# Performance work log

Hardware: AMD Instinct MI355X
Metric: run time of the kernel (lower is better)

## Reference

```python
import math
import jax, jax.numpy as jnp
import numpy as np

D_MODEL = 512
NHEAD = 8
D_HEAD = D_MODEL // NHEAD
TEMP = 0.8
B, LQ, LK = 16, 512, 1024
NEG = -1.0e9


def setup_inputs() -> dict:
    key = jax.random.key(0)
    ks = jax.random.split(key, 12)
    s = 1.0 / math.sqrt(D_MODEL)
    return {
        "Q_src": jax.random.normal(ks[0], (B, LQ, D_MODEL), jnp.float32),
        "KV_src": jax.random.normal(ks[1], (B, LK, D_MODEL), jnp.float32),
        "key_gate": jax.random.uniform(ks[2], (B, LK), jnp.float32, 1e-3, 1.0),
        "key_padding_mask": jax.random.randint(ks[3], (B, LK), 0, 2, jnp.int32),
        "Wq": jax.random.normal(ks[4], (D_MODEL, D_MODEL), jnp.float32) * s,
        "bq": jnp.zeros((D_MODEL,), jnp.float32),
        "Wk": jax.random.normal(ks[5], (D_MODEL, D_MODEL), jnp.float32) * s,
        "bk": jnp.zeros((D_MODEL,), jnp.float32),
        "Wv": jax.random.normal(ks[6], (D_MODEL, D_MODEL), jnp.float32) * s,
        "bv": jnp.zeros((D_MODEL,), jnp.float32),
        "Wo": jax.random.normal(ks[7], (D_MODEL, D_MODEL), jnp.float32) * s,
        "bo": jnp.zeros((D_MODEL,), jnp.float32),
    }


def reference(Q_src, KV_src, key_gate, key_padding_mask, Wq, bq, Wk, bk, Wv, bv, Wo, bo):
    b, lq, _ = Q_src.shape
    lk = KV_src.shape[1]
    # projections -> [B, H, L, Dh]
    q = (Q_src @ Wq + bq).reshape(b, lq, NHEAD, D_HEAD).transpose(0, 2, 1, 3)
    k = (KV_src @ Wk + bk).reshape(b, lk, NHEAD, D_HEAD).transpose(0, 2, 1, 3)
    v = (KV_src @ Wv + bv).reshape(b, lk, NHEAD, D_HEAD).transpose(0, 2, 1, 3)
    # scores with log-gate bias [B, H, Lq, Lk]
    logits = jnp.einsum("bhqd,bhkd->bhqk", q, k) / math.sqrt(D_HEAD)
    logits = logits + jnp.log(key_gate)[:, None, None, :]
    pad = (key_padding_mask == 0)[:, None, None, :]
    logits = jnp.where(pad, NEG, logits) / TEMP
    attn = jax.nn.softmax(logits, axis=-1)
    ctx = jnp.einsum("bhqk,bhkd->bhqd", attn, v)
    ctx = ctx.transpose(0, 2, 1, 3).reshape(b, lq, D_MODEL)
    return ctx @ Wo + bo
```

## Files before the change

kernel.cpp:

```cpp
#include <hip/hip_runtime.h>
#include <math.h>

typedef __bf16 bf16;
typedef __bf16 bf16x8 __attribute__((ext_vector_type(8)));
typedef __bf16 bf16x4 __attribute__((ext_vector_type(4)));
typedef __bf16 bf16x2 __attribute__((ext_vector_type(2)));
typedef float  f32x4  __attribute__((ext_vector_type(4)));
typedef unsigned int uint;

#define SCQ2 0.22542110f
#define SMREF 16.0f

#define VMC(n) asm volatile("s_waitcnt vmcnt(" #n ")" ::: "memory")
#define BARR do { __builtin_amdgcn_s_barrier(); __builtin_amdgcn_sched_barrier(0); } while (0)

#if __has_builtin(__builtin_amdgcn_exp2f)
#define EXP2F __builtin_amdgcn_exp2f
#else
#define EXP2F exp2f
#endif

__device__ __forceinline__ void gload16(const void* g, void* l) {
  __builtin_amdgcn_global_load_lds((const __attribute__((address_space(1))) void*)g,
                                   (__attribute__((address_space(3))) void*)l, 16, 0, 0);
}

__device__ __forceinline__ uint pk2(float a, float b) {
  bf16x2 t = {(bf16)a, (bf16)b};
  return __builtin_bit_cast(uint, t);
}

union V8 { bf16x8 v; bf16x4 h[2]; uint u[4]; };

__global__ void prep_k(const float* __restrict__ Wq, const float* __restrict__ Wk,
                       const float* __restrict__ Wv, const float* __restrict__ Wo,
                       bf16* __restrict__ Tq, bf16* __restrict__ Tkv, bf16* __restrict__ To,
                       const float* __restrict__ gate, const int* __restrict__ mask,
                       float* __restrict__ gfac,
                       const float* __restrict__ Qs, const float* __restrict__ KVs,
                       bf16* __restrict__ Qsb, bf16* __restrict__ KVb) {
  const int bid = blockIdx.x, tid = threadIdx.x;
  if (bid < 256) {
    const int w = bid >> 6, t = bid & 63;
    const float* W = (w == 0) ? Wq : (w == 1) ? Wk : (w == 2) ? Wv : Wo;
    bf16* T = (w == 0) ? Tq : (w == 3) ? To : Tkv;
    const int ro = (w == 2) ? 512 : 0;
    const int k0 = (t >> 3) * 64, n0 = (t & 7) * 64;
    __shared__ bf16 tl[64][72];
#pragma unroll
    for (int i = 0; i < 16; i++) {
      int s = i * 256 + tid;
      int r = s >> 6, c = s & 63;
      tl[r][c] = (bf16)W[(size_t)(k0 + r) * 512 + n0 + c];
    }
    __syncthreads();
#pragma unroll
    for (int i = 0; i < 16; i++) {
      int s = i * 256 + tid;
      int r = s >> 6, c = s & 63;
      T[(size_t)(ro + n0 + r) * 512 + k0 + c] = tl[c][r];
    }
  } else if (bid < 320) {
    int i = (bid - 256) * 256 + tid;
    gfac[i] = mask[i] ? __expf(1.25f * __logf(gate[i])) : 0.0f;
  } else {
    const float* s;
    bf16* d;
    size_t i;
    if (bid < 2368) { s = Qs; d = Qsb; i = ((size_t)(bid - 320) * 256 + tid) * 8; }
    else            { s = KVs; d = KVb; i = ((size_t)(bid - 2368) * 256 + tid) * 8; }
    f32x4 a = *(const f32x4*)(s + i);
    f32x4 b = *(const f32x4*)(s + i + 4);
    bf16x8 o = {(bf16)a[0], (bf16)a[1], (bf16)a[2], (bf16)a[3],
                (bf16)b[0], (bf16)b[1], (bf16)b[2], (bf16)b[3]};
    *(bf16x8*)(d + i) = o;
  }
}

__global__ __launch_bounds__(512, 2) void gemm_kv8(
    const bf16* __restrict__ A, const bf16* __restrict__ Bt,
    const float* __restrict__ kb, const float* __restrict__ vb,
    const float* __restrict__ gfac, bf16* __restrict__ K_out, bf16* __restrict__ V_out) {
  const int tid = threadIdx.x, w = tid >> 6, l = tid & 63;
  const int lg = l >> 4, lr = l & 15;
  const int bid = (int)(blockIdx.x & 7) * 32 + (int)(blockIdx.x >> 3);
  const int bm = (bid >> 2) * 256;
  const int bn = (bid & 3) * 256;
  const int wm = w >> 2, wn = w & 3;

  __shared__ __align__(16) bf16 AB[2][16384];

  const int lrow = l >> 2;
  const int cs = (l & 3) ^ ((l >> 3) & 3);

  f32x4 acc[8][4];
#pragma unroll
  for (int i = 0; i < 8; i++)
#pragma unroll
    for (int j = 0; j < 4; j++) acc[i][j] = (f32x4){0.f, 0.f, 0.f, 0.f};

  auto stA = [&](int p, int u, int kt) {
    const int rb = (w >> 2) * 128 + u * 64 + (w & 3) * 16;
    gload16(A + (size_t)(bm + rb + lrow) * 512 + kt * 32 + cs * 8, &AB[p][rb * 32]);
  };
  auto stB = [&](int p, int u, int kt) {
    const int rb = (w >> 1) * 64 + u * 32 + (w & 1) * 16;
    gload16(Bt + (size_t)(bn + rb + lrow) * 512 + kt * 32 + cs * 8, &AB[p][8192 + rb * 32]);
  };

  bf16x8 aA[4], bb0[2], bb1[2];
#define RDA(p, mh)                                                                   \
  _Pragma("unroll") for (int m2 = 0; m2 < 4; m2++) {                                 \
    const int row = wm * 128 + (mh) * 64 + m2 * 16 + lr;                             \
    aA[m2] = *(const bf16x8*)(&AB[p][row * 32 + ((lg ^ ((row >> 1) & 3)) * 8)]);     \
  }
#define RDB(p, nh, dst)                                                              \
  _Pragma("unroll") for (int n2 = 0; n2 < 2; n2++) {                                 \
    const int row = wn * 64 + (nh) * 32 + n2 * 16 + lr;                              \
    dst[n2] = *(const bf16x8*)(&AB[p][8192 + row * 32 + ((lg ^ ((row >> 1) & 3)) * 8)]); \
  }
#define MM(mh, nh, bbv)                                                              \
  __builtin_amdgcn_s_setprio(1);                                                     \
  _Pragma("unroll") for (int m2 = 0; m2 < 4; m2++)                                   \
  _Pragma("unroll") for (int n2 = 0; n2 < 2; n2++)                                   \
    acc[(mh) * 4 + m2][(nh) * 2 + n2] =                                              \
        __builtin_amdgcn_mfma_f32_16x16x32_bf16(aA[m2], bbv[n2],                     \
                                                acc[(mh) * 4 + m2][(nh) * 2 + n2], 0, 0, 0); \
  __builtin_amdgcn_s_setprio(0);

  stA(0, 0, 0); stB(0, 0, 0); stA(0, 1, 0); stB(0, 1, 0);
  stA(1, 0, 1); stB(1, 0, 1);
  VMC(4);
  BARR;

  for (int i = 0; i < 8; ++i) {
    const bool last = (i == 7);
    const int k1 = 2 * i + 1, k2 = 2 * i + 2, k3 = 2 * i + 3;
    stA(1, 1, k1); stB(1, 1, k1);
    RDA(0, 0); RDB(0, 0, bb0);
    MM(0, 0, bb0);
    VMC(4); BARR;
    RDB(0, 1, bb1);
    MM(0, 1, bb1);
    BARR;
    if (!last) stA(0, 0, k2);
    RDA(0, 1);
    MM(1, 0, bb0);
    BARR;
    if (!last) stB(0, 0, k2);
    MM(1, 1, bb1);
    if (last) { VMC(2); } else { VMC(4); }
    BARR;
    if (!last) { stA(0, 1, k2); stB(0, 1, k2); }
    RDA(1, 0); RDB(1, 0, bb0);
    MM(0, 0, bb0);
    if (last) { VMC(0); } else { VMC(4); }
    BARR;
    RDB(1, 1, bb1);
    MM(0, 1, bb1);
    BARR;
    if (!last) stA(1, 0, k3);
    RDA(1, 1);
    MM(1, 0, bb0);
    BARR;
    if (!last) stB(1, 0, k3);
    MM(1, 1, bb1);
    VMC(4); BARR;
  }
#undef RDA
#undef RDB
#undef MM

  if (bn < 512) {
#pragma unroll
    for (int mf = 0; mf < 8; mf++) {
#pragma unroll
      for (int nf = 0; nf < 4; nf++) {
        f32x4 c = acc[mf][nf];
        const int n = bn + wn * 64 + nf * 16 + lr;
        const int m0 = bm + wm * 128 + mf * 16 + lg * 4;
        const float bias = kb[n];
#pragma unroll
        for (int r = 0; r < 4; r++) K_out[(size_t)(m0 + r) * 512 + n] = (bf16)(c[r] + bias);
      }
    }
  } else {
#pragma unroll
    for (int mf = 0; mf < 8; mf++) {
#pragma unroll
      for (int nf = 0; nf < 4; nf++) {
        f32x4 c = acc[mf][nf];
        const int n = bn + wn * 64 + nf * 16 + lr;
        const int m0 = bm + wm * 128 + mf * 16 + lg * 4;
        const int nn = n - 512;
        const int hh = nn >> 6, dd = nn & 63;
        const int bb = m0 >> 10, key = m0 & 1023;
        const int u = key & 31;
        const int keyp = (key & ~31) + ((u & 15) >> 2) * 8 + ((u >> 4) & 1) * 4;
        const float bias = vb[nn];
        f32x4 g4 = *(const f32x4*)(gfac + m0);
        bf16x4 w4 = {(bf16)((c[0] + bias) * g4[0]), (bf16)((c[1] + bias) * g4[1]),
                     (bf16)((c[2] + bias) * g4[2]), (bf16)((c[3] + bias) * g4[3])};
        *(bf16x4*)(V_out + ((size_t)((bb * 8 + hh) * 64 + dd)) * 1024 + keyp) = w4;
      }
    }
  }
}

template <int OM, int NT, int CHUNK>
__global__ __launch_bounds__(256, 2) void gemm_k(
    const bf16* __restrict__ A, const bf16* __restrict__ Bt,
    const float* __restrict__ b0, void* __restrict__ C0, float scale) {
  const int tid = threadIdx.x, w = tid >> 6, l = tid & 63;
  const int lg = l >> 4, lr = l & 15;
  const int bid = (int)(blockIdx.x & 7) * CHUNK + (int)(blockIdx.x >> 3);
  const int bm = (bid / NT) * 64;
  const int bn = (bid % NT) * 128;
  const int wr = (w >> 1) * 32, wc = (w & 1) * 64;
  __shared__ __align__(16) bf16 As[3][64][32];
  __shared__ __align__(16) bf16 Bs[3][128][32];
  const int r16 = l >> 2;
  const int cs = (l & 3) ^ ((l >> 3) & 3);

  f32x4 acc[2][4];
#pragma unroll
  for (int i = 0; i < 2; i++)
#pragma unroll
    for (int j = 0; j < 4; j++) acc[i][j] = (f32x4){0.f, 0.f, 0.f, 0.f};

  auto stage = [&](int buf, int kt) {
    gload16(A + (size_t)(bm + w * 16 + r16) * 512 + kt * 32 + cs * 8, &As[buf][w * 16][0]);
#pragma unroll
    for (int j = 0; j < 2; j++)
      gload16(Bt + (size_t)(bn + w * 32 + j * 16 + r16) * 512 + kt * 32 + cs * 8,
              &Bs[buf][w * 32 + j * 16][0]);
  };

  stage(0, 0);
  stage(1, 1);
  for (int t = 0; t < 16; ++t) {
    const int buf = t % 3;
    if (t == 15) { VMC(0); } else { VMC(3); }
    BARR;
    if (t < 14) stage((t + 2) % 3, t + 2);
    bf16x8 af[2], bfr[4];
#pragma unroll
    for (int mf = 0; mf < 2; mf++) {
      const int row = wr + mf * 16 + lr;
      af[mf] = *(const bf16x8*)(&As[buf][row][(lg ^ ((row >> 1) & 3)) * 8]);
    }
#pragma unroll
    for (int nf = 0; nf < 4; nf++) {
      const int row = wc + nf * 16 + lr;
      bfr[nf] = *(const bf16x8*)(&Bs[buf][row][(lg ^ ((row >> 1) & 3)) * 8]);
    }
    __builtin_amdgcn_s_setprio(1);
#pragma unroll
    for (int mf = 0; mf < 2; mf++)
#pragma unroll
      for (int nf = 0; nf < 4; nf++)
        acc[mf][nf] = __builtin_amdgcn_mfma_f32_16x16x32_bf16(af[mf], bfr[nf], acc[mf][nf], 0, 0, 0);
    __builtin_amdgcn_s_setprio(0);
  }

#pragma unroll
  for (int mf = 0; mf < 2; mf++) {
#pragma unroll
    for (int nf = 0; nf < 4; nf++) {
      f32x4 c = acc[mf][nf];
      const int n = bn + wc + nf * 16 + lr;
      const int m0 = bm + wr + mf * 16 + lg * 4;
      const float bias = b0[n];
      if constexpr (OM == 0) {
        bf16* C = (bf16*)C0;
#pragma unroll
        for (int r = 0; r < 4; r++) C[(size_t)(m0 + r) * 512 + n] = (bf16)((c[r] + bias) * scale);
      } else {
        float* C = (float*)C0;
#pragma unroll
        for (int r = 0; r < 4; r++) C[(size_t)(m0 + r) * 512 + n] = c[r] + bias;
      }
    }
  }
}

__global__ __launch_bounds__(512, 1) void attn_k(
    const bf16* __restrict__ Q, const bf16* __restrict__ Kb,
    const bf16* __restrict__ Vt, const float* __restrict__ gfac,
    bf16* __restrict__ ctx) {
  const int tid = threadIdx.x, w = tid >> 6, l = tid & 63;
  const int lg = l >> 4, lr = l & 15;
  const int ks = w >> 2, wl = w & 3;
  const int bid = (int)(blockIdx.x & 7) * 32 + (int)(blockIdx.x >> 3);
  const int qb = bid & 1, h = (bid >> 1) & 7, b = bid >> 4;
  const int q0 = qb * 256;

  __shared__ __align__(16) bf16 Ks[2][2][64][64];
  __shared__ __align__(16) bf16 Vs[2][2][64][64];
  __shared__ __align__(16) float gfs[1024];

  bf16x8 qf[4][2];
#pragma unroll
  for (int s = 0; s < 4; s++) {
    const bf16* qp = Q + (size_t)(b * 512 + q0 + wl * 64 + s * 16 + lr) * 512 + h * 64;
    qf[s][0] = *(const bf16x8*)(qp + lg * 8);
    qf[s][1] = *(const bf16x8*)(qp + 32 + lg * 8);
  }

  f32x4 o[4][4];
#pragma unroll
  for (int s = 0; s < 4; s++)
#pragma unroll
    for (int i = 0; i < 4; i++) o[s][i] = (f32x4){0.f, 0.f, 0.f, 0.f};
  f32x4 lacc[4] = {(f32x4){0.f, 0.f, 0.f, 0.f}, (f32x4){0.f, 0.f, 0.f, 0.f},
                   (f32x4){0.f, 0.f, 0.f, 0.f}, (f32x4){0.f, 0.f, 0.f, 0.f}};

  const int r8 = l >> 3;
  const int c8g = (l & 7) ^ ((l >> 3) & 7);
  const bf16* Kbase = Kb + ((size_t)b * 1024) * 512 + h * 64 + c8g * 8;
  const bf16* Vbase = Vt + ((size_t)(b * 8 + h) * 64) * 1024 + c8g * 8;

  auto stage = [&](int buf, int t) {
    const int kv0 = ks * 512 + t * 64;
    gload16(Kbase + (size_t)(kv0 + wl * 16 + r8) * 512, &Ks[ks][buf][wl * 16][0]);
    gload16(Kbase + (size_t)(kv0 + wl * 16 + 8 + r8) * 512, &Ks[ks][buf][wl * 16 + 8][0]);
    gload16(Vbase + (size_t)(wl * 16 + r8) * 1024 + kv0, &Vs[ks][buf][wl * 16][0]);
    gload16(Vbase + (size_t)(wl * 16 + 8 + r8) * 1024 + kv0, &Vs[ks][buf][wl * 16 + 8][0]);
  };

  if (w < 4) gload16(gfac + b * 1024 + w * 256 + l * 4, &gfs[w * 256]);
  stage(0, 0);

  for (int t = 0; t < 8; ++t) {
    const int buf = t & 1;
    VMC(0);
    BARR;
    if (t < 7) stage(buf ^ 1, t + 1);

    f32x4 gvv[4];
#pragma unroll
    for (int f = 0; f < 4; f++)
      gvv[f] = *(const f32x4*)(&gfs[ks * 512 + t * 64 + f * 16 + lg * 4]);

    bf16x8 kf[4][2];
#pragma unroll
    for (int f = 0; f < 4; f++) {
      const int row = f * 16 + lr;
      kf[f][0] = *(const bf16x8*)(&Ks[ks][buf][row][(lg ^ (row & 7)) * 8]);
      kf[f][1] = *(const bf16x8*)(&Ks[ks][buf][row][((4 + lg) ^ (row & 7)) * 8]);
    }

    V8 pb[4][2];
#pragma unroll
    for (int s = 0; s < 4; s++) {
      f32x4 s4[4];
      __builtin_amdgcn_s_setprio(1);
#pragma unroll
      for (int f = 0; f < 4; f++) {
        f32x4 z = (f32x4){-SMREF, -SMREF, -SMREF, -SMREF};
        z = __builtin_amdgcn_mfma_f32_16x16x32_bf16(kf[f][0], qf[s][0], z, 0, 0, 0);
        s4[f] = __builtin_amdgcn_mfma_f32_16x16x32_bf16(kf[f][1], qf[s][1], z, 0, 0, 0);
      }
      __builtin_amdgcn_s_setprio(0);
      float p[4][4];
#pragma unroll
      for (int f = 0; f < 4; f++)
#pragma unroll
        for (int r = 0; r < 4; r++) p[f][r] = EXP2F(s4[f][r]);
#pragma unroll
      for (int f = 0; f < 4; f++)
#pragma unroll
        for (int r = 0; r < 4; r++) lacc[s][r] = fmaf(p[f][r], gvv[f][r], lacc[s][r]);
      pb[s][0].u[0] = pk2(p[0][0], p[0][1]); pb[s][0].u[1] = pk2(p[0][2], p[0][3]);
      pb[s][0].u[2] = pk2(p[1][0], p[1][1]); pb[s][0].u[3] = pk2(p[1][2], p[1][3]);
      pb[s][1].u[0] = pk2(p[2][0], p[2][1]); pb[s][1].u[1] = pk2(p[2][2], p[2][3]);
      pb[s][1].u[2] = pk2(p[3][0], p[3][1]); pb[s][1].u[3] = pk2(p[3][2], p[3][3]);
    }

    __builtin_amdgcn_s_setprio(1);
#pragma unroll
    for (int od = 0; od < 4; od++) {
      const int row = od * 16 + lr;
      const bf16x8 va0 = *(const bf16x8*)(&Vs[ks][buf][row][(lg ^ (row & 7)) * 8]);
      const bf16x8 va1 = *(const bf16x8*)(&Vs[ks][buf][row][((4 + lg) ^ (row & 7)) * 8]);
#pragma unroll
      for (int s = 0; s < 4; s++) {
        o[s][od] = __builtin_amdgcn_mfma_f32_16x16x32_bf16(va0, pb[s][0].v, o[s][od], 0, 0, 0);
        o[s][od] = __builtin_amdgcn_mfma_f32_16x16x32_bf16(va1, pb[s][1].v, o[s][od], 0, 0, 0);
      }
    }
    __builtin_amdgcn_s_setprio(0);
  }

  f32x4* OmA = (f32x4*)&Ks[0][0][0][0];
  f32x4* OmB = (f32x4*)&Vs[0][0][0][0];
  float* Lp = (float*)gfs;
  __syncthreads();
  if (ks == 1) {
    const int base = (wl * 64 + l) * 8;
#pragma unroll
    for (int s = 0; s < 2; s++)
#pragma unroll
      for (int od = 0; od < 4; od++) OmA[base + ((s * 4 + od) ^ (l & 7))] = o[s][od];
#pragma unroll
    for (int s = 2; s < 4; s++)
#pragma unroll
      for (int od = 0; od < 4; od++) OmB[base + (((s - 2) * 4 + od) ^ (l & 7))] = o[s][od];
#pragma unroll
    for (int s = 0; s < 4; s++)
      Lp[(wl * 64 + l) * 4 + s] = (lacc[s][0] + lacc[s][1]) + (lacc[s][2] + lacc[s][3]);
  }
  __syncthreads();
  if (ks == 0) {
    const int base = (wl * 64 + l) * 8;
#pragma unroll
    for (int s = 0; s < 2; s++)
#pragma unroll
      for (int od = 0; od < 4; od++) o[s][od] += OmA[base + ((s * 4 + od) ^ (l & 7))];
#pragma unroll
    for (int s = 2; s < 4; s++)
#pragma unroll
      for (int od = 0; od < 4; od++) o[s][od] += OmB[base + (((s - 2) * 4 + od) ^ (l & 7))];
#pragma unroll
    for (int s = 0; s < 4; s++) {
      float lp = (lacc[s][0] + lacc[s][1]) + (lacc[s][2] + lacc[s][3]) +
                 Lp[(wl * 64 + l) * 4 + s];
      lp += __shfl_xor(lp, 16);
      lp += __shfl_xor(lp, 32);
      const float inv = 1.0f / lp;
      bf16* cp = ctx + (size_t)(b * 512 + q0 + wl * 64 + s * 16 + lr) * 512 + h * 64;
#pragma unroll
      for (int od = 0; od < 4; od++)
#pragma unroll
        for (int r = 0; r < 4; r++) cp[od * 16 + lg * 4 + r] = (bf16)(o[s][od][r] * inv);
    }
  }
}

extern "C" void kernel_launch(void* const* d_in, const int* in_sizes, int n_in,
                              void* d_out, int out_size, void* d_ws, size_t ws_size,
                              hipStream_t stream) {
  (void)in_sizes; (void)n_in; (void)out_size; (void)ws_size;
  const float* Q_src = (const float*)d_in[0];
  const float* KV_src = (const float*)d_in[1];
  const float* gate = (const float*)d_in[2];
  const int* mask = (const int*)d_in[3];
  const float* Wq = (const float*)d_in[4];
  const float* bq = (const float*)d_in[5];
  const float* Wk = (const float*)d_in[6];
  const float* bk = (const float*)d_in[7];
  const float* Wv = (const float*)d_in[8];
  const float* bv = (const float*)d_in[9];
  const float* Wo = (const float*)d_in[10];
  const float* bo = (const float*)d_in[11];
  float* out = (float*)d_out;

  char* ws = (char*)d_ws;
  size_t off = 0;
  auto alloc = [&](size_t bytes) {
    char* p = ws + off;
    off += (bytes + 255) & ~(size_t)255;
    return p;
  };
  bf16* Wtq = (bf16*)alloc(512 * 512 * 2);
  bf16* Btkv = (bf16*)alloc(1024 * 512 * 2);
  bf16* Wto = (bf16*)alloc(512 * 512 * 2);
  float* gfac = (float*)alloc(16384 * 4);
  bf16* Qsb = (bf16*)alloc((size_t)8192 * 512 * 2);
  bf16* KVb = (bf16*)alloc((size_t)16384 * 512 * 2);
  bf16* Qb = (bf16*)alloc((size_t)8192 * 512 * 2);
  bf16* Kb = (bf16*)alloc((size_t)16384 * 512 * 2);
  bf16* Vt = (bf16*)alloc((size_t)16384 * 512 * 2);
  bf16* Cx = KVb;

  prep_k<<<6464, 256, 0, stream>>>(Wq, Wk, Wv, Wo, Wtq, Btkv, Wto, gate, mask, gfac,
                                   Q_src, KV_src, Qsb, KVb);
  gemm_kv8<<<256, 512, 0, stream>>>(KVb, Btkv, bk, bv, gfac, Kb, Vt);
  gemm_k<0, 4, 64><<<512, 256, 0, stream>>>(Qsb, Wtq, bq, Qb, SCQ2);
  attn_k<<<256, 512, 0, stream>>>(Qb, Kb, Vt, gfac, Cx);
  gemm_k<2, 4, 64><<<512, 256, 0, stream>>>(Cx, Wto, bo, out, 1.0f);
}
```

Before: 86.19 us.

## Load K/V fragments directly from global into registers, drop LDS staging

Removes the LDS double-buffered K/V staging with per-iteration barriers. Each wave now reads its K and V MFMA fragments straight from global memory into registers, with K prefetched one tile ahead and the gate factors also read from global. Launch bounds are changed to allow two blocks per CU. In exchange, the four query-row waves sharing a kv-split now each fetch the same K/V data, so traffic relies on L1/L2 hits, and register pressure rises from the doubled K buffer plus V fragments under the tighter launch bound.

```diff
diff --git a/kernel.cpp b/kernel.cpp
--- a/kernel.cpp
+++ b/kernel.cpp
@@ -284,7 +284,7 @@
   }
 }
 
-__global__ __launch_bounds__(512, 1) void attn_k(
+__global__ __launch_bounds__(512, 2) void attn_k(
     const bf16* __restrict__ Q, const bf16* __restrict__ Kb,
     const bf16* __restrict__ Vt, const float* __restrict__ gfac,
     bf16* __restrict__ ctx) {
@@ -295,9 +295,9 @@
   const int qb = bid & 1, h = (bid >> 1) & 7, b = bid >> 4;
   const int q0 = qb * 256;
 
-  __shared__ __align__(16) bf16 Ks[2][2][64][64];
-  __shared__ __align__(16) bf16 Vs[2][2][64][64];
-  __shared__ __align__(16) float gfs[1024];
+  __shared__ __align__(16) f32x4 OmA[2048];
+  __shared__ __align__(16) f32x4 OmB[2048];
+  __shared__ __align__(16) float Lp[1024];
 
   bf16x8 qf[4][2];
 #pragma unroll
@@ -315,40 +315,35 @@
   f32x4 lacc[4] = {(f32x4){0.f, 0.f, 0.f, 0.f}, (f32x4){0.f, 0.f, 0.f, 0.f},
                    (f32x4){0.f, 0.f, 0.f, 0.f}, (f32x4){0.f, 0.f, 0.f, 0.f}};
 
-  const int r8 = l >> 3;
-  const int c8g = (l & 7) ^ ((l >> 3) & 7);
-  const bf16* Kbase = Kb + ((size_t)b * 1024) * 512 + h * 64 + c8g * 8;
-  const bf16* Vbase = Vt + ((size_t)(b * 8 + h) * 64) * 1024 + c8g * 8;
-
-  auto stage = [&](int buf, int t) {
-    const int kv0 = ks * 512 + t * 64;
-    gload16(Kbase + (size_t)(kv0 + wl * 16 + r8) * 512, &Ks[ks][buf][wl * 16][0]);
-    gload16(Kbase + (size_t)(kv0 + wl * 16 + 8 + r8) * 512, &Ks[ks][buf][wl * 16 + 8][0]);
-    gload16(Vbase + (size_t)(wl * 16 + r8) * 1024 + kv0, &Vs[ks][buf][wl * 16][0]);
-    gload16(Vbase + (size_t)(wl * 16 + 8 + r8) * 1024 + kv0, &Vs[ks][buf][wl * 16 + 8][0]);
+  const bf16* Kbh = Kb + ((size_t)(b * 1024 + ks * 512)) * 512 + h * 64;
+  const bf16* Vbh = Vt + ((size_t)(b * 8 + h) * 64) * 1024 + ks * 512;
+  const float* gbh = gfac + b * 1024 + ks * 512;
+
+  bf16x8 kf[2][4][2];
+  auto loadK = [&](int t, int buf) {
+#pragma unroll
+    for (int f = 0; f < 4; f++) {
+      const size_t ro = (size_t)(t * 64 + f * 16 + lr) * 512;
+      kf[buf][f][0] = *(const bf16x8*)(Kbh + ro + lg * 8);
+      kf[buf][f][1] = *(const bf16x8*)(Kbh + ro + 32 + lg * 8);
+    }
   };
 
-  if (w < 4) gload16(gfac + b * 1024 + w * 256 + l * 4, &gfs[w * 256]);
-  stage(0, 0);
+  loadK(0, 0);
 
   for (int t = 0; t < 8; ++t) {
-    const int buf = t & 1;
-    VMC(0);
-    BARR;
-    if (t < 7) stage(buf ^ 1, t + 1);
-
+    const int cur = t & 1;
+    bf16x8 vf[4][2];
+#pragma unroll
+    for (int od = 0; od < 4; od++) {
+      const size_t ro = (size_t)(od * 16 + lr) * 1024 + t * 64;
+      vf[od][0] = *(const bf16x8*)(Vbh + ro + lg * 8);
+      vf[od][1] = *(const bf16x8*)(Vbh + ro + (4 + lg) * 8);
+    }
     f32x4 gvv[4];
 #pragma unroll
-    for (int f = 0; f < 4; f++)
-      gvv[f] = *(const f32x4*)(&gfs[ks * 512 + t * 64 + f * 16 + lg * 4]);
-
-    bf16x8 kf[4][2];
-#pragma unroll
-    for (int f = 0; f < 4; f++) {
-      const int row = f * 16 + lr;
-      kf[f][0] = *(const bf16x8*)(&Ks[ks][buf][row][(lg ^ (row & 7)) * 8]);
-      kf[f][1] = *(const bf16x8*)(&Ks[ks][buf][row][((4 + lg) ^ (row & 7)) * 8]);
-    }
+    for (int f = 0; f < 4; f++) gvv[f] = *(const f32x4*)(gbh + t * 64 + f * 16 + lg * 4);
+    if (t < 7) loadK(t + 1, cur ^ 1);
 
     V8 pb[4][2];
 #pragma unroll
@@ -358,8 +353,8 @@
 #pragma unroll
       for (int f = 0; f < 4; f++) {
         f32x4 z = (f32x4){-SMREF, -SMREF, -SMREF, -SMREF};
-        z = __builtin_amdgcn_mfma_f32_16x16x32_bf16(kf[f][0], qf[s][0], z, 0, 0, 0);
-        s4[f] = __builtin_amdgcn_mfma_f32_16x16x32_bf16(kf[f][1], qf[s][1], z, 0, 0, 0);
+        z = __builtin_amdgcn_mfma_f32_16x16x32_bf16(kf[cur][f][0], qf[s][0], z, 0, 0, 0);
+        s4[f] = __builtin_amdgcn_mfma_f32_16x16x32_bf16(kf[cur][f][1], qf[s][1], z, 0, 0, 0);
       }
       __builtin_amdgcn_s_setprio(0);
       float p[4][4];
@@ -380,21 +375,15 @@
     __builtin_amdgcn_s_setprio(1);
 #pragma unroll
     for (int od = 0; od < 4; od++) {
-      const int row = od * 16 + lr;
-      const bf16x8 va0 = *(const bf16x8*)(&Vs[ks][buf][row][(lg ^ (row & 7)) * 8]);
-      const bf16x8 va1 = *(const bf16x8*)(&Vs[ks][buf][row][((4 + lg) ^ (row & 7)) * 8]);
 #pragma unroll
       for (int s = 0; s < 4; s++) {
-        o[s][od] = __builtin_amdgcn_mfma_f32_16x16x32_bf16(va0, pb[s][0].v, o[s][od], 0, 0, 0);
-        o[s][od] = __builtin_amdgcn_mfma_f32_16x16x32_bf16(va1, pb[s][1].v, o[s][od], 0, 0, 0);
+        o[s][od] = __builtin_amdgcn_mfma_f32_16x16x32_bf16(vf[od][0], pb[s][0].v, o[s][od], 0, 0, 0);
+        o[s][od] = __builtin_amdgcn_mfma_f32_16x16x32_bf16(vf[od][1], pb[s][1].v, o[s][od], 0, 0, 0);
       }
     }
     __builtin_amdgcn_s_setprio(0);
   }
 
-  f32x4* OmA = (f32x4*)&Ks[0][0][0][0];
-  f32x4* OmB = (f32x4*)&Vs[0][0][0][0];
-  float* Lp = (float*)gfs;
   __syncthreads();
   if (ks == 1) {
     const int base = (wl * 64 + l) * 8;
```

Result: slower. 120.6 us (+39.9%).
